# Performance work log

Hardware: AMD Instinct MI355X
Metric: run time of the kernel (lower is better)

The kernel has to match this reference:

```python
import jax, jax.numpy as jnp
from jax import lax
import numpy as np

BATCH, T, IN_DIM, RES = 32, 2048, 64, 1024
SPECTRAL_RADIUS, SPARSITY, INPUT_SCALING, LEAK = 1.2, 0.2, 0.5, 0.3


def setup_inputs() -> dict:
    key = jax.random.key(0)
    inputs = jax.random.normal(key, (BATCH, T, IN_DIM), dtype=jnp.float32)
    # Replicate the layer's build(): fixed random reservoir, seeded numpy RNG.
    rng = np.random.RandomState(42)
    W_in = rng.uniform(-INPUT_SCALING, INPUT_SCALING, size=(IN_DIM, RES)).astype(np.float32)
    W_res = rng.randn(RES, RES)
    mask = rng.rand(RES, RES) < SPARSITY
    W_res *= mask
    sr = np.max(np.abs(np.linalg.eigvals(W_res)))
    if sr > 0:
        W_res *= SPECTRAL_RADIUS / sr
    return {
        "inputs": inputs,
        "W_in": jnp.asarray(W_in),
        "W_res": jnp.asarray(W_res.astype(np.float32)),
    }


def reference(inputs, W_in, W_res):
    # inputs: [B, T, I]; W_in: [I, R]; W_res: [R, R]
    leak = jnp.asarray(LEAK, inputs.dtype)
    # Hoist the input projection out of the recurrence (same math, one big GEMM).
    x_proj = jnp.einsum("bti,ir->btr", inputs, W_in)  # [B, T, R]
    state0 = jnp.zeros((inputs.shape[0], W_res.shape[0]), dtype=inputs.dtype)

    def step(state, x_t):  # x_t: [B, R]
        new_state = jnp.tanh(x_t + state @ W_res)
        state = (1.0 - leak) * state + leak * new_state
        return state, state

    _, states = lax.scan(step, state0, jnp.swapaxes(x_proj, 0, 1))  # [T, B, R]
    return jnp.swapaxes(states, 0, 1)  # [B, T, R] (return_sequences=True)
```

## Files before the change

kernel.cpp:

```cpp
#include <hip/hip_runtime.h>

#define T_STEPS 2048
#define NBATCH  32
#define IN_DIM  64
#define RES     1024
#define LEAKF   0.3f
#define NCG     64
#define NBG     4

typedef unsigned long long u64cp;

__global__ __launch_bounds__(256, 1) void esn_persist(
    const float* __restrict__ inp,
    const float* __restrict__ Win,
    const float* __restrict__ Wres,
    float* __restrict__ out,
    float* __restrict__ sC,
    unsigned* __restrict__ flags)
{
    const int tid   = threadIdx.x;
    const int c_loc = tid & 15;
    const int ks    = tid >> 4;
    const int cg    = blockIdx.x;
    const int bg    = blockIdx.y;
    const int c0    = cg * 16;
    const int b0    = bg * 8;
    const int c     = c0 + c_loc;

    float w[64];
    {
        const float* wp = Wres + (size_t)(ks * 64) * RES + c;
        #pragma unroll
        for (int j = 0; j < 64; ++j) w[j] = wp[(size_t)j * RES];
    }

    __shared__ __align__(16) float sst[8256];
    __shared__ float pl[16][8][17];

    unsigned* flg = flags + bg * NCG;
    float* sCb = sC + (size_t)bg * 2 * RES * 8;

    const int fb = tid >> 4;
    float s_prev = 0.f;

    for (int t = 0; t < T_STEPS; ++t) {
        float* sCr = sCb + ((t & 1) ^ 1) * (RES * 8);
        float* sCw = sCb + (t & 1) * (RES * 8);

        float x = 0.f;
        if (tid < 128) {
            const float* inb = inp + ((size_t)(b0 + fb) * T_STEPS + t) * IN_DIM;
            #pragma unroll
            for (int i = 0; i < IN_DIM; i += 4) {
                const float4 v = *reinterpret_cast<const float4*>(inb + i);
                x = fmaf(v.x, Win[(size_t)(i + 0) * RES + c], x);
                x = fmaf(v.y, Win[(size_t)(i + 1) * RES + c], x);
                x = fmaf(v.z, Win[(size_t)(i + 2) * RES + c], x);
                x = fmaf(v.w, Win[(size_t)(i + 3) * RES + c], x);
            }
        }

        if (t > 0) {
            if (tid < NCG) {
                const unsigned tgt = (unsigned)t;
                while (__hip_atomic_load(&flg[tid], __ATOMIC_RELAXED,
                                         __HIP_MEMORY_SCOPE_AGENT) < tgt) { }
            }
            __syncthreads();

            #pragma unroll
            for (int i = 0; i < 8; ++i) {
                const int m = i * 256 + tid;
                u64cp lo = __hip_atomic_load((u64cp*)(sCr + (size_t)m * 4),
                                             __ATOMIC_RELAXED, __HIP_MEMORY_SCOPE_AGENT);
                u64cp hi = __hip_atomic_load((u64cp*)(sCr + (size_t)m * 4 + 2),
                                             __ATOMIC_RELAXED, __HIP_MEMORY_SCOPE_AGENT);
                float4* dst = (float4*)((char*)sst + (size_t)m * 16 + (m >> 7) * 16);
                *dst = make_float4(__uint_as_float((unsigned)(lo       )),
                                   __uint_as_float((unsigned)(lo >> 32u)),
                                   __uint_as_float((unsigned)(hi       )),
                                   __uint_as_float((unsigned)(hi >> 32u)));
            }
            __syncthreads();
        }

        float acc0 = 0.f, acc1 = 0.f, acc2 = 0.f, acc3 = 0.f;
        float acc4 = 0.f, acc5 = 0.f, acc6 = 0.f, acc7 = 0.f;
        if (t > 0) {
            const char* base = (const char*)sst + (size_t)(ks * 64) * 32 + ks * 16;
            #pragma unroll
            for (int j = 0; j < 64; ++j) {
                const float4 sa = *reinterpret_cast<const float4*>(base + j * 32);
                const float4 sb = *reinterpret_cast<const float4*>(base + j * 32 + 16);
                const float wj = w[j];
                acc0 = fmaf(sa.x, wj, acc0);
                acc1 = fmaf(sa.y, wj, acc1);
                acc2 = fmaf(sa.z, wj, acc2);
                acc3 = fmaf(sa.w, wj, acc3);
                acc4 = fmaf(sb.x, wj, acc4);
                acc5 = fmaf(sb.y, wj, acc5);
                acc6 = fmaf(sb.z, wj, acc6);
                acc7 = fmaf(sb.w, wj, acc7);
            }
        }

        pl[ks][0][c_loc] = acc0;
        pl[ks][1][c_loc] = acc1;
        pl[ks][2][c_loc] = acc2;
        pl[ks][3][c_loc] = acc3;
        pl[ks][4][c_loc] = acc4;
        pl[ks][5][c_loc] = acc5;
        pl[ks][6][c_loc] = acc6;
        pl[ks][7][c_loc] = acc7;
        __syncthreads();

        if (tid < 128) {
            float sum = 0.f;
            #pragma unroll
            for (int q = 0; q < 16; ++q) sum += pl[q][fb][c_loc];

            const float nw = tanhf(x + sum);
            const float sn = fmaf(1.0f - LEAKF, s_prev, LEAKF * nw);
            s_prev = sn;

            out[((size_t)(b0 + fb) * T_STEPS + t) * RES + c] = sn;
            __hip_atomic_store(sCw + (size_t)c * 8 + fb, sn,
                               __ATOMIC_RELAXED, __HIP_MEMORY_SCOPE_AGENT);
        }
        __syncthreads();

        if (tid == 0)
            __hip_atomic_store(&flg[cg], (unsigned)(t + 1),
                               __ATOMIC_RELAXED, __HIP_MEMORY_SCOPE_AGENT);
    }
}

__global__ __launch_bounds__(256) void esn_step(
    const float* __restrict__ inp,
    const float* __restrict__ Win,
    const float* __restrict__ Wres,
    float* __restrict__ out,
    float* __restrict__ sT,
    int t)
{
    const int tid   = threadIdx.x;
    const int c_loc = tid & 15;
    const int ks    = tid >> 4;
    const int c0    = blockIdx.x * 16;
    const int b0    = blockIdx.y * 8;
    const int c     = c0 + c_loc;

    const float* sTr = sT + ((t & 1) ^ 1) * (RES * NBATCH);
    float*       sTw = sT + (t & 1) * (RES * NBATCH);

    float acc0 = 0.f, acc1 = 0.f, acc2 = 0.f, acc3 = 0.f;
    float acc4 = 0.f, acc5 = 0.f, acc6 = 0.f, acc7 = 0.f;

    if (t > 0) {
        const int kbeg = ks * 64;
        const float* wp = Wres + (size_t)kbeg * RES + c;
        const float* sp = sTr + kbeg * NBATCH + b0;
        #pragma unroll 4
        for (int j = 0; j < 64; ++j) {
            const float w = wp[(size_t)j * RES];
            const float4 sa = *reinterpret_cast<const float4*>(sp + j * NBATCH);
            const float4 sb = *reinterpret_cast<const float4*>(sp + j * NBATCH + 4);
            acc0 = fmaf(sa.x, w, acc0);
            acc1 = fmaf(sa.y, w, acc1);
            acc2 = fmaf(sa.z, w, acc2);
            acc3 = fmaf(sa.w, w, acc3);
            acc4 = fmaf(sb.x, w, acc4);
            acc5 = fmaf(sb.y, w, acc5);
            acc6 = fmaf(sb.z, w, acc6);
            acc7 = fmaf(sb.w, w, acc7);
        }
    }

    __shared__ float pl[16][8][17];
    pl[ks][0][c_loc] = acc0;
    pl[ks][1][c_loc] = acc1;
    pl[ks][2][c_loc] = acc2;
    pl[ks][3][c_loc] = acc3;
    pl[ks][4][c_loc] = acc4;
    pl[ks][5][c_loc] = acc5;
    pl[ks][6][c_loc] = acc6;
    pl[ks][7][c_loc] = acc7;
    __syncthreads();

    if (tid < 128) {
        const int b  = tid >> 4;
        const int cl = tid & 15;
        const int cgl = c0 + cl;
        const int bgl = b0 + b;

        float sum = 0.f;
        #pragma unroll
        for (int q = 0; q < 16; ++q) sum += pl[q][b][cl];

        const float* inb = inp + ((size_t)bgl * T_STEPS + t) * IN_DIM;
        float x = 0.f;
        #pragma unroll 8
        for (int i = 0; i < IN_DIM; ++i)
            x = fmaf(inb[i], Win[(size_t)i * RES + cgl], x);

        const float a  = x + sum;
        const float nw = tanhf(a);
        const float spv = (t > 0) ? sTr[cgl * NBATCH + bgl] : 0.f;
        const float sn = fmaf(1.0f - LEAKF, spv, LEAKF * nw);

        out[((size_t)bgl * T_STEPS + t) * RES + cgl] = sn;
        sTw[cgl * NBATCH + bgl] = sn;
    }
}

extern "C" void kernel_launch(void* const* d_in, const int* in_sizes, int n_in,
                              void* d_out, int out_size, void* d_ws, size_t ws_size,
                              hipStream_t stream)
{
    const float* inp  = (const float*)d_in[0];
    const float* Win  = (const float*)d_in[1];
    const float* Wres = (const float*)d_in[2];
    float* out = (float*)d_out;

    const size_t stateBytes = (size_t)NBG * 2 * RES * 8 * sizeof(float);
    const size_t flagBytes  = (size_t)NBG * NCG * sizeof(unsigned);

    if (ws_size >= stateBytes + flagBytes) {
        float* sC = (float*)d_ws;
        unsigned* flags = (unsigned*)((char*)d_ws + stateBytes);
        hipMemsetAsync(flags, 0, flagBytes, stream);
        hipLaunchKernelGGL(esn_persist, dim3(NCG, NBG), dim3(256), 0, stream,
                           inp, Win, Wres, out, sC, flags);
        return;
    }

    float* sT = (float*)d_ws;
    dim3 grid(64, 4), blk(256);
    for (int t = 0; t < T_STEPS; ++t) {
        hipLaunchKernelGGL(esn_step, grid, blk, 0, stream,
                           inp, Win, Wres, out, sT, t);
    }
}
```

Baseline: 21.18 ms.

## Replace flag barrier with per-element timestep-tagged state words

Each state value is now published as a 64-bit word that packs the timestep tag with the float, and readers poll each element until its tag matches the previous step. This removes the separate per-block flag array, the flag spin, and one __syncthreads per step. The aim is to cut inter-block synchronisation latency in the persistent recurrence. In exchange it doubles the state exchange traffic, and every thread now spins on 32 global words instead of a few threads spinning on 64 flags, which may add polling pressure on L2.

```diff
diff --git a/kernel.cpp b/kernel.cpp
--- a/kernel.cpp
+++ b/kernel.cpp
@@ -15,8 +15,7 @@
     const float* __restrict__ Win,
     const float* __restrict__ Wres,
     float* __restrict__ out,
-    float* __restrict__ sC,
-    unsigned* __restrict__ flags)
+    u64cp* __restrict__ tg)
 {
     const int tid   = threadIdx.x;
     const int c_loc = tid & 15;
@@ -37,15 +36,14 @@
     __shared__ __align__(16) float sst[8256];
     __shared__ float pl[16][8][17];
 
-    unsigned* flg = flags + bg * NCG;
-    float* sCb = sC + (size_t)bg * 2 * RES * 8;
+    u64cp* tgb = tg + (size_t)bg * 2 * RES * 8;
 
     const int fb = tid >> 4;
     float s_prev = 0.f;
 
     for (int t = 0; t < T_STEPS; ++t) {
-        float* sCr = sCb + ((t & 1) ^ 1) * (RES * 8);
-        float* sCw = sCb + (t & 1) * (RES * 8);
+        u64cp* tgr = tgb + ((t & 1) ^ 1) * (RES * 8);
+        u64cp* tgw = tgb + (t & 1) * (RES * 8);
 
         float x = 0.f;
         if (tid < 128) {
@@ -61,28 +59,28 @@
         }
 
         if (t > 0) {
-            if (tid < NCG) {
-                const unsigned tgt = (unsigned)t;
-                while (__hip_atomic_load(&flg[tid], __ATOMIC_RELAXED,
-                                         __HIP_MEMORY_SCOPE_AGENT) < tgt) { }
+            const unsigned expt = (unsigned)(t - 1);
+            const u64cp* tp = tgr + tid;
+            unsigned pend = 0xFFFFFFFFu;
+            while (pend) {
+                #pragma unroll
+                for (int j = 0; j < 32; ++j) {
+                    if (pend & (1u << j)) {
+                        const u64cp v = __hip_atomic_load(tp + j * 256,
+                                            __ATOMIC_RELAXED, __HIP_MEMORY_SCOPE_AGENT);
+                        if ((unsigned)(v >> 32) == expt) {
+                            const int idx = j * 256 + tid;
+                            const int k   = idx >> 3;
+                            const int b   = idx & 7;
+                            *(float*)((char*)sst + (size_t)k * 32 + ((k >> 6) * 16) + b * 4)
+                                = __uint_as_float((unsigned)v);
+                            pend &= ~(1u << j);
+                        }
+                    }
+                }
             }
-            __syncthreads();
-
-            #pragma unroll
-            for (int i = 0; i < 8; ++i) {
-                const int m = i * 256 + tid;
-                u64cp lo = __hip_atomic_load((u64cp*)(sCr + (size_t)m * 4),
-                                             __ATOMIC_RELAXED, __HIP_MEMORY_SCOPE_AGENT);
-                u64cp hi = __hip_atomic_load((u64cp*)(sCr + (size_t)m * 4 + 2),
-                                             __ATOMIC_RELAXED, __HIP_MEMORY_SCOPE_AGENT);
-                float4* dst = (float4*)((char*)sst + (size_t)m * 16 + (m >> 7) * 16);
-                *dst = make_float4(__uint_as_float((unsigned)(lo       )),
-                                   __uint_as_float((unsigned)(lo >> 32u)),
-                                   __uint_as_float((unsigned)(hi       )),
-                                   __uint_as_float((unsigned)(hi >> 32u)));
-            }
-            __syncthreads();
-        }
+        }
+        __syncthreads();
 
         float acc0 = 0.f, acc1 = 0.f, acc2 = 0.f, acc3 = 0.f;
         float acc4 = 0.f, acc5 = 0.f, acc6 = 0.f, acc7 = 0.f;
@@ -124,14 +122,10 @@
             s_prev = sn;
 
             out[((size_t)(b0 + fb) * T_STEPS + t) * RES + c] = sn;
-            __hip_atomic_store(sCw + (size_t)c * 8 + fb, sn,
+            const u64cp word = ((u64cp)(unsigned)t << 32) | (u64cp)__float_as_uint(sn);
+            __hip_atomic_store(tgw + (size_t)c * 8 + fb, word,
                                __ATOMIC_RELAXED, __HIP_MEMORY_SCOPE_AGENT);
         }
-        __syncthreads();
-
-        if (tid == 0)
-            __hip_atomic_store(&flg[cg], (unsigned)(t + 1),
-                               __ATOMIC_RELAXED, __HIP_MEMORY_SCOPE_AGENT);
     }
 }
 
@@ -222,15 +216,13 @@
     const float* Wres = (const float*)d_in[2];
     float* out = (float*)d_out;
 
-    const size_t stateBytes = (size_t)NBG * 2 * RES * 8 * sizeof(float);
-    const size_t flagBytes  = (size_t)NBG * NCG * sizeof(unsigned);
-
-    if (ws_size >= stateBytes + flagBytes) {
-        float* sC = (float*)d_ws;
-        unsigned* flags = (unsigned*)((char*)d_ws + stateBytes);
-        hipMemsetAsync(flags, 0, flagBytes, stream);
+    const size_t tagBytes = (size_t)NBG * 2 * RES * 8 * sizeof(u64cp);
+
+    if (ws_size >= tagBytes) {
+        u64cp* tg = (u64cp*)d_ws;
+        hipMemsetAsync(tg, 0xFF, tagBytes, stream);
         hipLaunchKernelGGL(esn_persist, dim3(NCG, NBG), dim3(256), 0, stream,
-                           inp, Win, Wres, out, sC, flags);
+                           inp, Win, Wres, out, tg);
         return;
     }
 
```

Result: slower. 39.51 ms (+86.5%).
